# Kernel optimization log

Hardware: AMD Instinct MI355X
Metric: run time of the kernel (lower is better)

The kernel has to match this reference:

```python
import jax, jax.numpy as jnp
import numpy as np

# ---- config (mirrors conf dict passed to RegionLoss.__init__) ----
ANCHORS = jnp.array([[1.3221, 1.73145], [3.19275, 4.00944], [5.05587, 8.09892],
                     [9.47112, 4.84053], [11.2364, 10.0071]], dtype=jnp.float32)
NUM_CLASSES = 80
OBJECT_SCALE = 5.0
NO_OBJECT_SCALE = 1.0
CLASS_SCALE = 1.0
COORD_SCALE = 1.0
SIL_THRESH = 0.6
SEEN = 0  # fresh module -> seen < 12800 warm-start branch is active


def _iou_center(a, b):
    """IoU of center-format boxes (cx, cy, w, h); a, b broadcastable [..., 4]."""
    ax1, ax2 = a[..., 0] - a[..., 2] * 0.5, a[..., 0] + a[..., 2] * 0.5
    ay1, ay2 = a[..., 1] - a[..., 3] * 0.5, a[..., 1] + a[..., 3] * 0.5
    bx1, bx2 = b[..., 0] - b[..., 2] * 0.5, b[..., 0] + b[..., 2] * 0.5
    by1, by2 = b[..., 1] - b[..., 3] * 0.5, b[..., 1] + b[..., 3] * 0.5
    iw = jnp.maximum(jnp.minimum(ax2, bx2) - jnp.maximum(ax1, bx1), 0.0)
    ih = jnp.maximum(jnp.minimum(ay2, by2) - jnp.maximum(ay1, by1), 0.0)
    inter = iw * ih
    union = a[..., 2] * a[..., 3] + b[..., 2] * b[..., 3] - inter
    return inter / union


def setup_inputs() -> dict:
    key = jax.random.key(0)
    k1, k2, k3, k4 = jax.random.split(key, 4)
    B, A, C, H, W, NBOX = 32, 5, NUM_CLASSES, 52, 52, 50
    pred = jax.random.normal(k1, (B, A * (C + 5), H, W), dtype=jnp.float32)
    cls = jax.random.randint(k2, (B, NBOX, 1), 0, C).astype(jnp.float32)
    xy = jax.random.uniform(k3, (B, NBOX, 2), minval=0.02, maxval=0.98, dtype=jnp.float32)
    wh = jax.random.uniform(k4, (B, NBOX, 2), minval=0.05, maxval=0.4, dtype=jnp.float32)
    target = jnp.concatenate([cls, xy, wh], axis=-1)  # (B, NBOX, 5): cls,x,y,w,h in [0,1]
    return {"pred": pred, "target": target, "train_out": 0}


def _region_loss(pred, target):
    B, H, W = pred.shape[0], pred.shape[2], pred.shape[3]
    A, C = ANCHORS.shape[0], NUM_CLASSES
    nbox = target.shape[1]
    p = pred.reshape(B, A, C + 5, H, W)

    txy = jax.nn.sigmoid(p[:, :, 0:2])                 # (B,A,2,H,W)
    twh = p[:, :, 2:4]                                 # (B,A,2,H,W)
    pred_no_off = jnp.concatenate([txy, twh], axis=2)  # (B,A,4,H,W)
    pred_conf = jax.nn.sigmoid(p[:, :, 4])             # (B,A,H,W)
    cls_logits = p[:, :, 5:]                           # (B,A,C,H,W)

    # decode boxes to grid units (detached in the original)
    grid_x = jnp.arange(W, dtype=p.dtype)              # broadcasts along W (last dim)
    grid_y = jnp.arange(H, dtype=p.dtype)[:, None]     # broadcasts along H
    aw = ANCHORS[:, 0][None, :, None, None]
    ah = ANCHORS[:, 1][None, :, None, None]
    bx = txy[:, :, 0] + grid_x
    by = txy[:, :, 1] + grid_y
    bw = jnp.exp(twh[:, :, 0]) * aw
    bh = jnp.exp(twh[:, :, 1]) * ah
    pred_boxes = jax.lax.stop_gradient(jnp.stack([bx, by, bw, bh], axis=-1))  # (B,A,H,W,4)

    # ground truth in grid units
    scale = jnp.array([W, H, W, H], dtype=p.dtype)
    gt = target[:, :, 1:5] * scale                     # (B,nbox,4) center format
    valid = target[:, :, 1] > 0                        # sentinel: x == 0 terminates

    # conf mask: zero-out cells whose best IoU vs any GT exceeds sil_thresh
    pb_flat = pred_boxes.reshape(B, A * H * W, 4)
    ious = _iou_center(gt[:, :, None, :], pb_flat[:, None, :, :])  # (B,nbox,A*H*W)
    ious = jnp.where(valid[:, :, None], ious, 0.0)
    max_iou = jnp.max(ious, axis=1).reshape(B, A, H, W)
    conf_mask = jnp.where(max_iou > SIL_THRESH, 0.0, NO_OBJECT_SCALE)

    # best anchor per GT via width/height-only IoU (boxes at origin)
    gw, gh = gt[..., 2], gt[..., 3]
    inter = jnp.minimum(gw[..., None], ANCHORS[:, 0]) * jnp.minimum(gh[..., None], ANCHORS[:, 1])
    union = gw[..., None] * gh[..., None] + ANCHORS[:, 0] * ANCHORS[:, 1] - inter
    best_a = jnp.argmax(inter / union, axis=-1)        # (B,nbox)

    gi = jnp.clip(gt[..., 0].astype(jnp.int32), 0, W - 1)
    gj = jnp.clip(gt[..., 1].astype(jnp.int32), 0, H - 1)
    b_idx = jnp.broadcast_to(jnp.arange(B)[:, None], (B, nbox))
    bi = jnp.where(valid, b_idx, B)                    # invalid GTs -> OOB batch, dropped

    aw_b = ANCHORS[best_a, 0]
    ah_b = ANCHORS[best_a, 1]
    tx_t = gt[..., 0] - gi.astype(p.dtype)
    ty_t = gt[..., 1] - gj.astype(p.dtype)
    tw_t = jnp.log(gw / aw_b)
    th_t = jnp.log(gh / ah_b)

    pred_box_at = pred_boxes[b_idx, best_a, gj, gi]    # (B,nbox,4) decoded box at GT cell
    iou_gt = _iou_center(gt, pred_box_at)              # (B,nbox)

    # initialize targets/masks (seen < 12800 warm start)
    if SEEN < 12800:
        coord_mask = jnp.ones((B, A, H, W), dtype=p.dtype)
        target_box = jnp.zeros((B, A, 4, H, W), dtype=p.dtype).at[:, :, 0:2].set(0.5)
    else:
        coord_mask = jnp.zeros((B, A, H, W), dtype=p.dtype)
        target_box = jnp.zeros((B, A, 4, H, W), dtype=p.dtype)
    cls_mask = jnp.zeros((B, A, H, W), dtype=p.dtype)
    target_conf = jnp.zeros((B, A, H, W), dtype=p.dtype)
    target_cls = jnp.zeros((B, A, H, W), dtype=p.dtype)

    coord_mask = coord_mask.at[bi, best_a, gj, gi].set(1.0, mode='drop')
    cls_mask = cls_mask.at[bi, best_a, gj, gi].set(1.0, mode='drop')
    conf_mask = conf_mask.at[bi, best_a, gj, gi].set(OBJECT_SCALE, mode='drop')
    target_box = target_box.at[bi, best_a, 0, gj, gi].set(tx_t, mode='drop')
    target_box = target_box.at[bi, best_a, 1, gj, gi].set(ty_t, mode='drop')
    target_box = target_box.at[bi, best_a, 2, gj, gi].set(tw_t, mode='drop')
    target_box = target_box.at[bi, best_a, 3, gj, gi].set(th_t, mode='drop')
    target_conf = target_conf.at[bi, best_a, gj, gi].set(iou_gt, mode='drop')
    target_cls = target_cls.at[bi, best_a, gj, gi].set(target[:, :, 0], mode='drop')

    # losses
    half = jnp.asarray(0.5, p.dtype)
    loss_x = COORD_SCALE * jnp.sum(((pred_no_off[:, :, 0] - target_box[:, :, 0]) * coord_mask) ** 2) * half
    loss_y = COORD_SCALE * jnp.sum(((pred_no_off[:, :, 1] - target_box[:, :, 1]) * coord_mask) ** 2) * half
    loss_w = COORD_SCALE * jnp.sum(((pred_no_off[:, :, 2] - target_box[:, :, 2]) * coord_mask) ** 2) * half
    loss_h = COORD_SCALE * jnp.sum(((pred_no_off[:, :, 3] - target_box[:, :, 3]) * coord_mask) ** 2) * half
    loss_conf = jnp.sum(((pred_conf - target_conf) * jnp.sqrt(conf_mask)) ** 2) * half

    logp = jax.nn.log_softmax(cls_logits, axis=2)      # (B,A,C,H,W)
    tcls = jnp.clip(target_cls.astype(jnp.int32), 0, C - 1)
    ce = -jnp.take_along_axis(logp, tcls[:, :, None], axis=2)[:, :, 0]  # (B,A,H,W)
    loss_cls = CLASS_SCALE * jnp.sum(cls_mask * ce)

    loss = loss_x + loss_y + loss_w + loss_h + loss_conf + loss_cls
    return loss, loss_x, loss_y, loss_w, loss_h, loss_conf, loss_cls


def reference(pred, target, train_out):
    out = _region_loss(pred, target)
    if train_out:
        return out
    return out[0]
```

## Files before the change

kernel.cpp:

```cpp
#include <hip/hip_runtime.h>
#include <math.h>

#define BB 32
#define AA 5
#define CC 80
#define HH 52
#define WW 52
#define NBOX 50
#define HWSZ (HH*WW)
#define CELLS (AA*HWSZ)

__constant__ float d_aw[AA] = {1.3221f, 3.19275f, 5.05587f, 9.47112f, 11.2364f};
__constant__ float d_ah[AA] = {1.73145f, 4.00944f, 8.09892f, 4.84053f, 10.0071f};

__device__ __forceinline__ float sig(float x) { return 1.f / (1.f + expf(-x)); }


__device__ __forceinline__ void cell_of(const float* t, int& best, int& gi, int& gj, float& valid) {
    float gx = t[1] * (float)WW;
    float gy = t[2] * (float)HH;
    float gw = t[3] * (float)WW;
    float gh = t[4] * (float)HH;
    valid = (t[1] > 0.f) ? 1.f : 0.f;
    best = 0; float bestv = -1.f;
    #pragma unroll
    for (int a = 0; a < AA; ++a) {
        float inter = fminf(gw, d_aw[a]) * fminf(gh, d_ah[a]);
        float uni = gw * gh + d_aw[a] * d_ah[a] - inter;
        float r = inter / uni;
        if (r > bestv) { bestv = r; best = a; }
    }
    gi = (int)gx; gi = gi < 0 ? 0 : (gi > WW - 1 ? WW - 1 : gi);
    gj = (int)gy; gj = gj < 0 ? 0 : (gj > HH - 1 ? HH - 1 : gj);
}

__global__ void region_prep(const float* __restrict__ pred,
                            const float* __restrict__ target,
                            float4* __restrict__ boxws) {
    int b = blockIdx.x;
    int j = threadIdx.x;
    if (j >= NBOX) return;
    const float* t = target + ((size_t)b * NBOX + j) * 5;
    float gx = t[1] * (float)WW;
    float gy = t[2] * (float)HH;
    float gw = t[3] * (float)WW;
    float gh = t[4] * (float)HH;
    int best, gi, gj; float valid;
    cell_of(t, best, gi, gj, valid);

    float tx_t = gx - (float)gi;
    float ty_t = gy - (float)gj;
    float tw_t = logf(gw / d_aw[best]);
    float th_t = logf(gh / d_ah[best]);

    size_t base = ((size_t)(b * AA + best) * (CC + 5)) * HWSZ + (size_t)gj * WW + gi;
    float px = sig(pred[base]) + (float)gi;
    float py = sig(pred[base + HWSZ]) + (float)gj;
    float pw = expf(pred[base + 2 * HWSZ]) * d_aw[best];
    float ph = expf(pred[base + 3 * HWSZ]) * d_ah[best];

    float ax1 = gx - gw * 0.5f, ax2 = gx + gw * 0.5f;
    float ay1 = gy - gh * 0.5f, ay2 = gy + gh * 0.5f;
    float bx1 = px - pw * 0.5f, bx2 = px + pw * 0.5f;
    float by1 = py - ph * 0.5f, by2 = py + ph * 0.5f;
    float iw = fmaxf(fminf(ax2, bx2) - fmaxf(ax1, bx1), 0.f);
    float ih = fmaxf(fminf(ay2, by2) - fmaxf(ay1, by1), 0.f);
    float inter = iw * ih;
    float iou_gt = inter / (gw * gh + pw * ph - inter);

    float is_last = 1.f;
    for (int j2 = j + 1; j2 < NBOX; ++j2) {
        const float* t2 = target + ((size_t)b * NBOX + j2) * 5;
        int b2, i2, jj2; float v2;
        cell_of(t2, b2, i2, jj2, v2);
        if (v2 != 0.f && b2 == best && i2 == gi && jj2 == gj) is_last = 0.f;
    }

    float4* o = boxws + ((size_t)b * NBOX + j) * 4;
    if (valid != 0.f) {
        o[0] = make_float4(ax1, ax2, ay1, ay2);
        o[1] = make_float4(gw * gh, (float)best, (float)gi, (float)gj);
    } else {
        o[0] = make_float4(0.f, 0.f, 0.f, 0.f);
        o[1] = make_float4(0.f, -1.f, -1.f, -1.f);
    }
    o[2] = make_float4(tx_t, ty_t, tw_t, th_t);
    o[3] = make_float4(iou_gt, t[0], valid, is_last);
}

__device__ __forceinline__ float wave_max(float v) {
    #pragma unroll
    for (int off = 32; off > 0; off >>= 1) v = fmaxf(v, __shfl_xor(v, off, 64));
    return v;
}
__device__ __forceinline__ float wave_sum(float v) {
    #pragma unroll
    for (int off = 32; off > 0; off >>= 1) v += __shfl_xor(v, off, 64);
    return v;
}

__global__ __launch_bounds__(256) void region_ce(const float* __restrict__ pred,
                                                 const float4* __restrict__ boxws,
                                                 float* __restrict__ out) {
    int b = blockIdx.x;
    int wave = threadIdx.x >> 6;
    int lane = threadIdx.x & 63;
    float acc = 0.f;
    for (int j = wave; j < NBOX; j += 4) {
        const float4* r = boxws + ((size_t)b * NBOX + j) * 4;
        float4 r1 = r[1];
        float4 r3 = r[3];
        if (r3.z == 0.f || r3.w == 0.f) continue;
        int a = (int)r1.y, gi = (int)r1.z, gj = (int)r1.w;
        size_t cbase = ((size_t)(b * AA + a) * (CC + 5) + 5) * HWSZ + (size_t)gj * WW + gi;
        float v1 = pred[cbase + (size_t)lane * HWSZ];
        float v2 = (lane < CC - 64) ? pred[cbase + (size_t)(lane + 64) * HWSZ] : -INFINITY;
        float mx = wave_max(fmaxf(v1, v2));
        float s = expf(v1 - mx) + ((lane < CC - 64) ? expf(v2 - mx) : 0.f);
        s = wave_sum(s);
        int tcls = (int)r3.y;
        tcls = tcls < 0 ? 0 : (tcls > CC - 1 ? CC - 1 : tcls);
        float vt = ((lane == tcls) ? v1 : 0.f) + ((lane + 64 == tcls) ? v2 : 0.f);
        vt = wave_sum(vt);
        if (lane == 0) acc += (mx + logf(s)) - vt;
    }
    if (lane == 0 && acc != 0.f) atomicAdd(out, acc);
}

__global__ __launch_bounds__(256) void region_loss(const float* __restrict__ pred,
                                                   const float4* __restrict__ boxws,
                                                   float* __restrict__ out) {
    __shared__ float4 sh[NBOX * 4];
    __shared__ float wsum[4];
    int b = blockIdx.y;
    int tid = threadIdx.x;
    if (tid < NBOX * 4) sh[tid] = boxws[(size_t)b * NBOX * 4 + tid];
    __syncthreads();

    int c = blockIdx.x * 256 + tid;
    float lsum = 0.f;
    if (c < CELLS) {
        int a = c / HWSZ;
        int rem = c - a * HWSZ;
        int hh = rem / WW;
        int wwi = rem - hh * WW;
        size_t base = ((size_t)(b * AA + a) * (CC + 5)) * HWSZ + rem;
        float p0 = pred[base];
        float p1 = pred[base + HWSZ];
        float p2 = pred[base + 2 * HWSZ];
        float p3 = pred[base + 3 * HWSZ];
        float p4 = pred[base + 4 * HWSZ];
        float tx = sig(p0);
        float ty = sig(p1);
        float conf = sig(p4);
        float bx = tx + (float)wwi;
        float by = ty + (float)hh;
        float bw = expf(p2) * d_aw[a];
        float bh = expf(p3) * d_ah[a];
        float px1 = bx - bw * 0.5f, px2 = bx + bw * 0.5f;
        float py1 = by - bh * 0.5f, py2 = by + bh * 0.5f;
        float parea = bw * bh;
        float af = (float)a, wf = (float)wwi, hf = (float)hh;

        float maxiou = 0.f;
        int win = -1;
        #pragma unroll 2
        for (int j = 0; j < NBOX; ++j) {
            float4 r0 = sh[j * 4 + 0];
            float4 r1 = sh[j * 4 + 1];
            float iw = fmaxf(fminf(px2, r0.y) - fmaxf(px1, r0.x), 0.f);
            float ih = fmaxf(fminf(py2, r0.w) - fmaxf(py1, r0.z), 0.f);
            float inter = iw * ih;
            float iou = inter / (parea + r1.x - inter);
            maxiou = fmaxf(maxiou, iou);
            bool m = (r1.y == af) & (r1.z == wf) & (r1.w == hf);
            win = m ? j : win;
        }

        float dx, dy, dw, dh, lconf;
        if (win >= 0) {
            float4 r2 = sh[win * 4 + 2];
            float4 r3 = sh[win * 4 + 3];
            dx = tx - r2.x; dy = ty - r2.y; dw = p2 - r2.z; dh = p3 - r2.w;
            float d = conf - r3.x;
            lconf = 2.5f * d * d;
        } else {
            dx = tx - 0.5f; dy = ty - 0.5f; dw = p2; dh = p3;
            float cm = (maxiou > 0.6f) ? 0.f : 1.f;
            lconf = 0.5f * cm * conf * conf;
        }
        lsum = 0.5f * (dx * dx + dy * dy + dw * dw + dh * dh) + lconf;
    }

    #pragma unroll
    for (int off = 32; off > 0; off >>= 1)
        lsum += __shfl_down(lsum, off, 64);
    int wave = tid >> 6;
    if ((tid & 63) == 0) wsum[wave] = lsum;
    __syncthreads();
    if (tid == 0) {
        atomicAdd(out, wsum[0] + wsum[1] + wsum[2] + wsum[3]);
    }
}

extern "C" void kernel_launch(void* const* d_in, const int* in_sizes, int n_in,
                              void* d_out, int out_size, void* d_ws, size_t ws_size,
                              hipStream_t stream) {
    const float* pred = (const float*)d_in[0];
    const float* target = (const float*)d_in[1];
    float* out = (float*)d_out;
    float4* boxws = (float4*)d_ws;

    hipMemsetAsync(out, 0, sizeof(float) * out_size, stream);
    region_prep<<<dim3(BB), dim3(64), 0, stream>>>(pred, target, boxws);
    region_ce<<<dim3(BB), dim3(256), 0, stream>>>(pred, boxws, out);
    dim3 grid((CELLS + 255) / 256, BB);
    region_loss<<<grid, dim3(256), 0, stream>>>(pred, boxws, out);
}
```

Before: 249.1 us.

## Fuse prep, cross-entropy and cell loss into a single kernel

Folds the three kernels into one. Each block recomputes the per-box targets into shared memory, so the workspace round-trip and two launches go away. The winning cell itself computes the class cross-entropy serially over the 80 logits, and the O(N^2) is_last scan is replaced by a last-match-wins cell index compare. The cost is redundant box prep in every block (about 52 blocks per batch) and a serial 80-logit, three-pass loop on a few divergent threads. The is_last check is dropped, and last-match-wins over a packed linear cell index should give the same winner.

```diff
diff --git a/kernel.cpp b/kernel.cpp
--- a/kernel.cpp
+++ b/kernel.cpp
@@ -15,129 +15,64 @@
 
 __device__ __forceinline__ float sig(float x) { return 1.f / (1.f + expf(-x)); }
 
+__global__ __launch_bounds__(256) void region_fused(const float* __restrict__ pred,
+                                                    const float* __restrict__ target,
+                                                    float* __restrict__ out) {
+    __shared__ float4 s_box[NBOX];
+    __shared__ float2 s_ac[NBOX];
+    __shared__ float4 s_t[NBOX];
+    __shared__ float2 s_m[NBOX];
+    __shared__ float wsum[4];
 
-__device__ __forceinline__ void cell_of(const float* t, int& best, int& gi, int& gj, float& valid) {
-    float gx = t[1] * (float)WW;
-    float gy = t[2] * (float)HH;
-    float gw = t[3] * (float)WW;
-    float gh = t[4] * (float)HH;
-    valid = (t[1] > 0.f) ? 1.f : 0.f;
-    best = 0; float bestv = -1.f;
-    #pragma unroll
-    for (int a = 0; a < AA; ++a) {
-        float inter = fminf(gw, d_aw[a]) * fminf(gh, d_ah[a]);
-        float uni = gw * gh + d_aw[a] * d_ah[a] - inter;
-        float r = inter / uni;
-        if (r > bestv) { bestv = r; best = a; }
+    const int b = blockIdx.y;
+    const int tid = threadIdx.x;
+
+    if (tid < NBOX) {
+        const float* t = target + ((size_t)b * NBOX + tid) * 5;
+        float t0 = t[0], t1 = t[1], t2 = t[2], t3 = t[3], t4 = t[4];
+        float gx = t1 * (float)WW, gy = t2 * (float)HH;
+        float gw = t3 * (float)WW, gh = t4 * (float)HH;
+        bool valid = t1 > 0.f;
+        int best = 0; float bestv = -1.f;
+        #pragma unroll
+        for (int a = 0; a < AA; ++a) {
+            float inter = fminf(gw, d_aw[a]) * fminf(gh, d_ah[a]);
+            float uni = gw * gh + d_aw[a] * d_ah[a] - inter;
+            float r = inter / uni;
+            if (r > bestv) { bestv = r; best = a; }
+        }
+        int gi = (int)gx; gi = gi < 0 ? 0 : (gi > WW - 1 ? WW - 1 : gi);
+        int gj = (int)gy; gj = gj < 0 ? 0 : (gj > HH - 1 ? HH - 1 : gj);
+
+        size_t bbase = ((size_t)(b * AA + best) * (CC + 5)) * HWSZ + (size_t)gj * WW + gi;
+        float px = sig(pred[bbase]) + (float)gi;
+        float py = sig(pred[bbase + HWSZ]) + (float)gj;
+        float pw = expf(pred[bbase + 2 * HWSZ]) * d_aw[best];
+        float ph = expf(pred[bbase + 3 * HWSZ]) * d_ah[best];
+
+        float ax1 = gx - gw * 0.5f, ax2 = gx + gw * 0.5f;
+        float ay1 = gy - gh * 0.5f, ay2 = gy + gh * 0.5f;
+        float bx1 = px - pw * 0.5f, bx2 = px + pw * 0.5f;
+        float by1 = py - ph * 0.5f, by2 = py + ph * 0.5f;
+        float iw = fmaxf(fminf(ax2, bx2) - fmaxf(ax1, bx1), 0.f);
+        float ih = fmaxf(fminf(ay2, by2) - fmaxf(ay1, by1), 0.f);
+        float inter = iw * ih;
+        float iou_gt = inter / (gw * gh + pw * ph - inter);
+
+        if (valid) {
+            s_box[tid] = make_float4(ax1, ax2, ay1, ay2);
+            s_ac[tid]  = make_float2(gw * gh, (float)(best * HWSZ + gj * WW + gi));
+        } else {
+            s_box[tid] = make_float4(0.f, 0.f, 0.f, 0.f);
+            s_ac[tid]  = make_float2(0.f, -1.f);
+        }
+        s_t[tid] = make_float4(gx - (float)gi, gy - (float)gj,
+                               logf(gw / d_aw[best]), logf(gh / d_ah[best]));
+        s_m[tid] = make_float2(iou_gt, t0);
     }
-    gi = (int)gx; gi = gi < 0 ? 0 : (gi > WW - 1 ? WW - 1 : gi);
-    gj = (int)gy; gj = gj < 0 ? 0 : (gj > HH - 1 ? HH - 1 : gj);
-}
-
-__global__ void region_prep(const float* __restrict__ pred,
-                            const float* __restrict__ target,
-                            float4* __restrict__ boxws) {
-    int b = blockIdx.x;
-    int j = threadIdx.x;
-    if (j >= NBOX) return;
-    const float* t = target + ((size_t)b * NBOX + j) * 5;
-    float gx = t[1] * (float)WW;
-    float gy = t[2] * (float)HH;
-    float gw = t[3] * (float)WW;
-    float gh = t[4] * (float)HH;
-    int best, gi, gj; float valid;
-    cell_of(t, best, gi, gj, valid);
-
-    float tx_t = gx - (float)gi;
-    float ty_t = gy - (float)gj;
-    float tw_t = logf(gw / d_aw[best]);
-    float th_t = logf(gh / d_ah[best]);
-
-    size_t base = ((size_t)(b * AA + best) * (CC + 5)) * HWSZ + (size_t)gj * WW + gi;
-    float px = sig(pred[base]) + (float)gi;
-    float py = sig(pred[base + HWSZ]) + (float)gj;
-    float pw = expf(pred[base + 2 * HWSZ]) * d_aw[best];
-    float ph = expf(pred[base + 3 * HWSZ]) * d_ah[best];
-
-    float ax1 = gx - gw * 0.5f, ax2 = gx + gw * 0.5f;
-    float ay1 = gy - gh * 0.5f, ay2 = gy + gh * 0.5f;
-    float bx1 = px - pw * 0.5f, bx2 = px + pw * 0.5f;
-    float by1 = py - ph * 0.5f, by2 = py + ph * 0.5f;
-    float iw = fmaxf(fminf(ax2, bx2) - fmaxf(ax1, bx1), 0.f);
-    float ih = fmaxf(fminf(ay2, by2) - fmaxf(ay1, by1), 0.f);
-    float inter = iw * ih;
-    float iou_gt = inter / (gw * gh + pw * ph - inter);
-
-    float is_last = 1.f;
-    for (int j2 = j + 1; j2 < NBOX; ++j2) {
-        const float* t2 = target + ((size_t)b * NBOX + j2) * 5;
-        int b2, i2, jj2; float v2;
-        cell_of(t2, b2, i2, jj2, v2);
-        if (v2 != 0.f && b2 == best && i2 == gi && jj2 == gj) is_last = 0.f;
-    }
-
-    float4* o = boxws + ((size_t)b * NBOX + j) * 4;
-    if (valid != 0.f) {
-        o[0] = make_float4(ax1, ax2, ay1, ay2);
-        o[1] = make_float4(gw * gh, (float)best, (float)gi, (float)gj);
-    } else {
-        o[0] = make_float4(0.f, 0.f, 0.f, 0.f);
-        o[1] = make_float4(0.f, -1.f, -1.f, -1.f);
-    }
-    o[2] = make_float4(tx_t, ty_t, tw_t, th_t);
-    o[3] = make_float4(iou_gt, t[0], valid, is_last);
-}
-
-__device__ __forceinline__ float wave_max(float v) {
-    #pragma unroll
-    for (int off = 32; off > 0; off >>= 1) v = fmaxf(v, __shfl_xor(v, off, 64));
-    return v;
-}
-__device__ __forceinline__ float wave_sum(float v) {
-    #pragma unroll
-    for (int off = 32; off > 0; off >>= 1) v += __shfl_xor(v, off, 64);
-    return v;
-}
-
-__global__ __launch_bounds__(256) void region_ce(const float* __restrict__ pred,
-                                                 const float4* __restrict__ boxws,
-                                                 float* __restrict__ out) {
-    int b = blockIdx.x;
-    int wave = threadIdx.x >> 6;
-    int lane = threadIdx.x & 63;
-    float acc = 0.f;
-    for (int j = wave; j < NBOX; j += 4) {
-        const float4* r = boxws + ((size_t)b * NBOX + j) * 4;
-        float4 r1 = r[1];
-        float4 r3 = r[3];
-        if (r3.z == 0.f || r3.w == 0.f) continue;
-        int a = (int)r1.y, gi = (int)r1.z, gj = (int)r1.w;
-        size_t cbase = ((size_t)(b * AA + a) * (CC + 5) + 5) * HWSZ + (size_t)gj * WW + gi;
-        float v1 = pred[cbase + (size_t)lane * HWSZ];
-        float v2 = (lane < CC - 64) ? pred[cbase + (size_t)(lane + 64) * HWSZ] : -INFINITY;
-        float mx = wave_max(fmaxf(v1, v2));
-        float s = expf(v1 - mx) + ((lane < CC - 64) ? expf(v2 - mx) : 0.f);
-        s = wave_sum(s);
-        int tcls = (int)r3.y;
-        tcls = tcls < 0 ? 0 : (tcls > CC - 1 ? CC - 1 : tcls);
-        float vt = ((lane == tcls) ? v1 : 0.f) + ((lane + 64 == tcls) ? v2 : 0.f);
-        vt = wave_sum(vt);
-        if (lane == 0) acc += (mx + logf(s)) - vt;
-    }
-    if (lane == 0 && acc != 0.f) atomicAdd(out, acc);
-}
-
-__global__ __launch_bounds__(256) void region_loss(const float* __restrict__ pred,
-                                                   const float4* __restrict__ boxws,
-                                                   float* __restrict__ out) {
-    __shared__ float4 sh[NBOX * 4];
-    __shared__ float wsum[4];
-    int b = blockIdx.y;
-    int tid = threadIdx.x;
-    if (tid < NBOX * 4) sh[tid] = boxws[(size_t)b * NBOX * 4 + tid];
     __syncthreads();
 
-    int c = blockIdx.x * 256 + tid;
+    const int c = blockIdx.x * 256 + tid;
     float lsum = 0.f;
     if (c < CELLS) {
         int a = c / HWSZ;
@@ -160,36 +95,45 @@
         float px1 = bx - bw * 0.5f, px2 = bx + bw * 0.5f;
         float py1 = by - bh * 0.5f, py2 = by + bh * 0.5f;
         float parea = bw * bh;
-        float af = (float)a, wf = (float)wwi, hf = (float)hh;
+        float cf = (float)c;
 
         float maxiou = 0.f;
         int win = -1;
         #pragma unroll 2
         for (int j = 0; j < NBOX; ++j) {
-            float4 r0 = sh[j * 4 + 0];
-            float4 r1 = sh[j * 4 + 1];
-            float iw = fmaxf(fminf(px2, r0.y) - fmaxf(px1, r0.x), 0.f);
-            float ih = fmaxf(fminf(py2, r0.w) - fmaxf(py1, r0.z), 0.f);
-            float inter = iw * ih;
-            float iou = inter / (parea + r1.x - inter);
+            float4 r0 = s_box[j];
+            float2 r1 = s_ac[j];
+            float iw2 = fmaxf(fminf(px2, r0.y) - fmaxf(px1, r0.x), 0.f);
+            float ih2 = fmaxf(fminf(py2, r0.w) - fmaxf(py1, r0.z), 0.f);
+            float inter2 = iw2 * ih2;
+            float iou = inter2 / (parea + r1.x - inter2);
             maxiou = fmaxf(maxiou, iou);
-            bool m = (r1.y == af) & (r1.z == wf) & (r1.w == hf);
-            win = m ? j : win;
+            win = (r1.y == cf) ? j : win;
         }
 
         float dx, dy, dw, dh, lconf;
         if (win >= 0) {
-            float4 r2 = sh[win * 4 + 2];
-            float4 r3 = sh[win * 4 + 3];
+            float4 r2 = s_t[win];
+            float2 r3 = s_m[win];
             dx = tx - r2.x; dy = ty - r2.y; dw = p2 - r2.z; dh = p3 - r2.w;
             float d = conf - r3.x;
             lconf = 2.5f * d * d;
+            int tcls = (int)r3.y;
+            tcls = tcls < 0 ? 0 : (tcls > CC - 1 ? CC - 1 : tcls);
+            const float* lg = pred + base + 5 * (size_t)HWSZ;
+            float mx = -INFINITY;
+            #pragma unroll 8
+            for (int cc = 0; cc < CC; ++cc) mx = fmaxf(mx, lg[(size_t)cc * HWSZ]);
+            float s = 0.f;
+            #pragma unroll 8
+            for (int cc = 0; cc < CC; ++cc) s += expf(lg[(size_t)cc * HWSZ] - mx);
+            lsum += (mx + logf(s)) - lg[(size_t)tcls * HWSZ];
         } else {
             dx = tx - 0.5f; dy = ty - 0.5f; dw = p2; dh = p3;
             float cm = (maxiou > 0.6f) ? 0.f : 1.f;
             lconf = 0.5f * cm * conf * conf;
         }
-        lsum = 0.5f * (dx * dx + dy * dy + dw * dw + dh * dh) + lconf;
+        lsum += 0.5f * (dx * dx + dy * dy + dw * dw + dh * dh) + lconf;
     }
 
     #pragma unroll
@@ -209,11 +153,8 @@
     const float* pred = (const float*)d_in[0];
     const float* target = (const float*)d_in[1];
     float* out = (float*)d_out;
-    float4* boxws = (float4*)d_ws;
 
     hipMemsetAsync(out, 0, sizeof(float) * out_size, stream);
-    region_prep<<<dim3(BB), dim3(64), 0, stream>>>(pred, target, boxws);
-    region_ce<<<dim3(BB), dim3(256), 0, stream>>>(pred, boxws, out);
     dim3 grid((CELLS + 255) / 256, BB);
-    region_loss<<<grid, dim3(256), 0, stream>>>(pred, boxws, out);
+    region_fused<<<grid, dim3(256), 0, stream>>>(pred, target, out);
 }
```

New measurement: 232.2 us. 6.8% less time.
